# Optimization experiments

Hardware: AMD Instinct MI355X
Metric: run time of the kernel (lower is better)

Reference implementation:

```python
import jax, jax.numpy as jnp
import numpy as np

V, E, H, L = 10000, 300, 256, 9   # vocab, embed_dim, hidden_dim, num_labels
B, T = 128, 512                   # batch, seq_len


def setup_inputs() -> dict:
    key = jax.random.key(0)
    ks = jax.random.split(key, 14)
    s = 0.05
    emb = jax.random.normal(ks[2], (V, E), jnp.float32) * s
    emb = emb.at[0].set(0.0)  # padding_idx=0
    return {
        "input_ids": jax.random.randint(ks[0], (B, T), 0, V),
        "attention_mask": jnp.ones((B, T), jnp.int32),
        "labels": jax.random.randint(ks[1], (B, T), 0, L),
        "emb": emb,
        "Wih_f": jax.random.normal(ks[3], (4 * H, E), jnp.float32) * s,
        "Whh_f": jax.random.normal(ks[4], (4 * H, H), jnp.float32) * s,
        "b_f": jnp.zeros((4 * H,), jnp.float32),
        "Wih_b": jax.random.normal(ks[5], (4 * H, E), jnp.float32) * s,
        "Whh_b": jax.random.normal(ks[6], (4 * H, H), jnp.float32) * s,
        "b_b": jnp.zeros((4 * H,), jnp.float32),
        "Wc": jax.random.normal(ks[7], (L, 2 * H), jnp.float32) * s,
        "bc": jnp.zeros((L,), jnp.float32),
        "transitions": jax.random.normal(ks[8], (L, L), jnp.float32) * 0.1,
        "start_trans": jax.random.normal(ks[9], (L,), jnp.float32) * 0.1,
        "end_trans": jax.random.normal(ks[10], (L,), jnp.float32) * 0.1,
    }


def _lstm_dir(x, Wih, Whh, b):
    # x: (T, B, E) -> hidden states (T, B, H); PyTorch gate order i,f,g,o
    Bn = x.shape[1]
    h0 = jnp.zeros((Bn, Whh.shape[1]), x.dtype)
    c0 = jnp.zeros((Bn, Whh.shape[1]), x.dtype)
    # precompute input projections once (big GEMM), scan only does small HxH GEMM
    xp = jnp.einsum('tbe,ge->tbg', x, Wih) + b
    def step(carry, xg):
        h, c = carry
        g = xg + h @ Whh.T
        i, f, gg, o = jnp.split(g, 4, axis=-1)
        c = jax.nn.sigmoid(f) * c + jax.nn.sigmoid(i) * jnp.tanh(gg)
        h = jax.nn.sigmoid(o) * jnp.tanh(c)
        return (h, c), h
    _, hs = jax.lax.scan(step, (h0, c0), xp)
    return hs


def reference(input_ids, attention_mask, labels, emb, Wih_f, Whh_f, b_f,
              Wih_b, Whh_b, b_b, Wc, bc, transitions, start_trans, end_trans):
    x = emb[input_ids]                       # (B, T, E)
    xt = jnp.transpose(x, (1, 0, 2))         # (T, B, E)
    hf = _lstm_dir(xt, Wih_f, Whh_f, b_f)
    hb = _lstm_dir(xt[::-1], Wih_b, Whh_b, b_b)[::-1]
    h = jnp.concatenate([hf, hb], axis=-1)   # (T, B, 2H); dropout is identity in eval
    em = h @ Wc.T + bc                       # (T, B, L) emissions

    mask = jnp.transpose(attention_mask, (1, 0)).astype(bool)  # (T, B)
    tags = jnp.transpose(labels, (1, 0))                        # (T, B)
    Bn = em.shape[1]
    bidx = jnp.arange(Bn)

    # --- numerator: score of gold path (torchcrf._compute_score) ---
    score0 = start_trans[tags[0]] + em[0, bidx, tags[0]]
    def num_step(carry, inp):
        score, prev = carry
        e_t, t_t, m_t = inp
        score = score + (transitions[prev, t_t] + e_t[bidx, t_t]) * m_t
        return (score, t_t), None
    (score, _), _ = jax.lax.scan(
        num_step, (score0, tags[0]),
        (em[1:], tags[1:], mask[1:].astype(em.dtype)))
    seq_ends = mask.astype(jnp.int32).sum(0) - 1
    last_tags = tags[seq_ends, bidx]
    score = score + end_trans[last_tags]

    # --- denominator: log partition (torchcrf._compute_normalizer) ---
    alpha0 = start_trans + em[0]             # (B, L)
    def den_step(alpha, inp):
        e_t, m_t = inp
        nxt = jax.nn.logsumexp(alpha[:, :, None] + transitions[None] + e_t[:, None, :], axis=1)
        return jnp.where(m_t[:, None], nxt, alpha), None
    alpha, _ = jax.lax.scan(den_step, alpha0, (em[1:], mask[1:]))
    logZ = jax.nn.logsumexp(alpha + end_trans, axis=-1)

    llh = score - logZ
    return -jnp.mean(llh)  # crf(..., reduction='mean'), negated
```

## Files before the change

### kernel.cpp

```cpp
#include <hip/hip_runtime.h>
#include <hip/hip_bf16.h>
#include <hip/hip_fp16.h>

#define Vn 10000
#define En 300
#define E2n 150
#define Hn 256
#define Gn 1024
#define Ln 9
#define Bn 128
#define Tn 512

#if defined(__has_builtin)
#  if __has_builtin(__builtin_amdgcn_sdot8)
#    define HAS_SDOT8 1
#  endif
#  if __has_builtin(__builtin_amdgcn_fdot2)
#    define HAS_FDOT2 1
#  endif
#endif
#ifndef HAS_SDOT8
#  define HAS_SDOT8 0
#endif
#ifndef HAS_FDOT2
#  define HAS_FDOT2 0
#endif

typedef _Float16 half2_t __attribute__((ext_vector_type(2)));

static __device__ __forceinline__ float bf2f(unsigned short u) {
    return __uint_as_float(((unsigned int)u) << 16);
}
static __device__ __forceinline__ unsigned short f2bf(float f) {
    unsigned int x = __float_as_uint(f);
    return (unsigned short)((x + 0x7FFFu + ((x >> 16) & 1u)) >> 16);
}
static __device__ __forceinline__ float sigm(float x) {
    return 1.f / (1.f + __expf(-x));
}
static __device__ __forceinline__ float tanh_fast(float x) {
    return 2.f / (1.f + __expf(-2.f * x)) - 1.f;
}
static __device__ __forceinline__ int dot8(unsigned int w, int h, int acc) {
#if HAS_SDOT8
    return __builtin_amdgcn_sdot8((int)w, h, acc, false);
#else
    unsigned int wl = ((w & 0x0F0F0F0Fu) ^ 0x08080808u) - 0x08080808u;
    unsigned int wh = (((w >> 4) & 0x0F0F0F0Fu) ^ 0x08080808u) - 0x08080808u;
    unsigned int hl = (((unsigned)h & 0x0F0F0F0Fu) ^ 0x08080808u) - 0x08080808u;
    unsigned int hh = ((((unsigned)h >> 4) & 0x0F0F0F0Fu) ^ 0x08080808u) - 0x08080808u;
    acc = __builtin_amdgcn_sdot4((int)wl, (int)hl, acc, false);
    return __builtin_amdgcn_sdot4((int)wh, (int)hh, acc, false);
#endif
}
static __device__ __forceinline__ float fdot2f(unsigned int a, unsigned int b, float acc) {
#if HAS_FDOT2
    return __builtin_amdgcn_fdot2(__builtin_bit_cast(half2_t, a),
                                  __builtin_bit_cast(half2_t, b), acc, false);
#else
    half2_t av = __builtin_bit_cast(half2_t, a);
    half2_t bv = __builtin_bit_cast(half2_t, b);
    return acc + (float)av.x * (float)bv.x + (float)av.y * (float)bv.y;
#endif
}
static __device__ __forceinline__ unsigned int packf16(float a, float b) {
    half2_t v = {(_Float16)a, (_Float16)b};
    return __builtin_bit_cast(unsigned int, v);
}

__global__ __launch_bounds__(256) void k_prep_emb(
    const float* __restrict__ emb, unsigned int* __restrict__ embp) {
    int n = blockIdx.x * 256 + threadIdx.x;
    if (n >= Vn * E2n) return;
    int v = n / E2n, e2 = n % E2n;
    float a = emb[(size_t)v * En + 2 * e2];
    float b = emb[(size_t)v * En + 2 * e2 + 1];
    embp[n] = packf16(a, b);
}

__global__ __launch_bounds__(256) void k_prep_wt(
    const float* __restrict__ Wf, const float* __restrict__ Wb,
    unsigned int* __restrict__ Tf, unsigned int* __restrict__ Tb) {
    int n = blockIdx.x * 256 + threadIdx.x;
    const float* src = blockIdx.y ? Wb : Wf;
    unsigned int* dst = blockIdx.y ? Tb : Tf;
    int e2 = n / Gn, j = n % Gn;
    float a = src[(size_t)j * En + 2 * e2];
    float b = src[(size_t)j * En + 2 * e2 + 1];
    dst[n] = packf16(a, b);
}

__global__ __launch_bounds__(64) void k_quant_whh(
    const float* __restrict__ Wf, const float* __restrict__ Wb,
    unsigned int* __restrict__ qr_f, unsigned int* __restrict__ ql_f,
    unsigned int* __restrict__ qr_b, unsigned int* __restrict__ ql_b,
    float* __restrict__ scl_f, float* __restrict__ scl_b) {
    int j = blockIdx.x;
    int dir = blockIdx.y;
    int lane = threadIdx.x;
    const float* W = dir ? Wb : Wf;
    float w8[8];
    float m = 0.f;
    if (lane < 32) {
        float4 wlo = *(const float4*)&W[(size_t)j * Hn + 8 * lane];
        float4 whi = *(const float4*)&W[(size_t)j * Hn + 8 * lane + 4];
        w8[0] = wlo.x; w8[1] = wlo.y; w8[2] = wlo.z; w8[3] = wlo.w;
        w8[4] = whi.x; w8[5] = whi.y; w8[6] = whi.z; w8[7] = whi.w;
        #pragma unroll
        for (int i = 0; i < 8; ++i) m = fmaxf(m, fabsf(w8[i]));
    }
    #pragma unroll
    for (int sft = 32; sft >= 1; sft >>= 1) m = fmaxf(m, __shfl_xor(m, sft, 64));
    float inv = (m > 0.f) ? (7.f / m) : 0.f;
    if (lane < 32) {
        unsigned int d = 0;
        #pragma unroll
        for (int i = 0; i < 8; ++i) {
            int qi = (int)rintf(w8[i] * inv);
            d |= ((unsigned int)(qi & 0xF)) << (4 * i);
        }
        if (lane < 16)
            (dir ? qr_b : qr_f)[(size_t)((lane >> 2) * 1024 + j) * 4 + (lane & 3)] = d;
        else {
            int e = lane - 16;
            (dir ? ql_b : ql_f)[(size_t)((e >> 2) * 1024 + j) * 4 + (e & 3)] = d;
        }
    }
    if (lane == 0) (dir ? scl_b : scl_f)[j] = m / 49.f;
}

__global__ __launch_bounds__(256) void k_proj(
    const unsigned int* __restrict__ embp,
    const unsigned int* __restrict__ WT16_f, const unsigned int* __restrict__ WT16_b,
    const float* __restrict__ b_f, const float* __restrict__ b_b,
    unsigned short* __restrict__ Pf, unsigned short* __restrict__ Pb) {
    int tid = threadIdx.x;
    int tx = tid & 63, ty = tid >> 6;
    int dir = blockIdx.z;
    const unsigned int* WT = dir ? WT16_b : WT16_f;
    const float* bias = dir ? b_b : b_f;
    unsigned short* P = dir ? Pb : Pf;
    int v0 = blockIdx.x * 32 + ty * 8;
    int j0 = blockIdx.y * 256 + tx * 4;
    int vr[8];
    #pragma unroll
    for (int r = 0; r < 8; ++r) { int v = v0 + r; vr[r] = (v < Vn) ? v : Vn - 1; }
    float4 acc[8];
    #pragma unroll
    for (int r = 0; r < 8; ++r) acc[r] = make_float4(0.f, 0.f, 0.f, 0.f);
    for (int e2 = 0; e2 < E2n; ++e2) {
        uint4 w = *(const uint4*)&WT[(size_t)e2 * Gn + j0];
        #pragma unroll
        for (int r = 0; r < 8; ++r) {
            unsigned int a = embp[(size_t)vr[r] * E2n + e2];
            acc[r].x = fdot2f(a, w.x, acc[r].x);
            acc[r].y = fdot2f(a, w.y, acc[r].y);
            acc[r].z = fdot2f(a, w.z, acc[r].z);
            acc[r].w = fdot2f(a, w.w, acc[r].w);
        }
    }
    float4 bb = *(const float4*)&bias[j0];
    #pragma unroll
    for (int r = 0; r < 8; ++r) {
        if (v0 + r < Vn) {
            ushort4 o;
            o.x = f2bf(acc[r].x + bb.x); o.y = f2bf(acc[r].y + bb.y);
            o.z = f2bf(acc[r].z + bb.z); o.w = f2bf(acc[r].w + bb.w);
            *(ushort4*)&P[(size_t)(v0 + r) * Gn + j0] = o;
        }
    }
}

__global__ __launch_bounds__(1024, 4) void k_lstm(
    const int* __restrict__ ids,
    const uint4* __restrict__ qr_f, const uint4* __restrict__ ql_f,
    const uint4* __restrict__ qr_b, const uint4* __restrict__ ql_b,
    const float* __restrict__ scl_f, const float* __restrict__ scl_b,
    const unsigned short* __restrict__ Pf, const unsigned short* __restrict__ Pb,
    unsigned short* __restrict__ hs_f, unsigned short* __restrict__ hs_b) {
    __shared__ uint4 wlds[4 * 1024];
    __shared__ float g_stage[Gn];
    __shared__ uint4 h4v[8];
    __shared__ int ids_lds[Tn];
    int tid = threadIdx.x;
    int dir = blockIdx.x >> 7;
    int batch = blockIdx.x & 127;
    const uint4* qr = dir ? qr_b : qr_f;
    const uint4* ql = dir ? ql_b : ql_f;
    const unsigned short* P = dir ? Pb : Pf;
    unsigned short* hs = dir ? hs_b : hs_f;

    unsigned int wReg[16];
    #pragma unroll
    for (int d4 = 0; d4 < 4; ++d4) {
        uint4 v = qr[(size_t)d4 * 1024 + tid];
        wReg[4*d4+0] = v.x; wReg[4*d4+1] = v.y; wReg[4*d4+2] = v.z; wReg[4*d4+3] = v.w;
        wlds[d4 * 1024 + tid] = ql[(size_t)d4 * 1024 + tid];
    }
    float sc = (dir ? scl_b : scl_f)[tid];
    if (tid < Tn) ids_lds[tid] = ids[batch * Tn + tid];
    if (tid < 8) { uint4 z = {0u, 0u, 0u, 0u}; h4v[tid] = z; }
    float c = 0.f;
    __syncthreads();

    int t0 = dir ? (Tn - 1) : 0;
    float p = bf2f(P[(size_t)ids_lds[t0] * Gn + tid]);

    for (int s = 0; s < Tn; ++s) {
        asm volatile("" : "+v"(wReg[0]), "+v"(wReg[1]), "+v"(wReg[2]), "+v"(wReg[3]),
                          "+v"(wReg[4]), "+v"(wReg[5]), "+v"(wReg[6]), "+v"(wReg[7]),
                          "+v"(wReg[8]), "+v"(wReg[9]), "+v"(wReg[10]), "+v"(wReg[11]),
                          "+v"(wReg[12]), "+v"(wReg[13]), "+v"(wReg[14]), "+v"(wReg[15]));

        int t = dir ? (Tn - 1 - s) : s;
        int s2 = (s + 1 < Tn) ? s + 1 : Tn - 1;
        int t2 = dir ? (Tn - 1 - s2) : s2;
        unsigned short nx = P[(size_t)ids_lds[t2] * Gn + tid];

        uint4 hq  = h4v[tid & 7];
        uint4 wv0 = wlds[tid];
        uint4 wv1 = wlds[1024 + tid];
        uint4 wv2 = wlds[2048 + tid];
        uint4 wv3 = wlds[3072 + tid];

        int a0 = 0, a1 = 0, a2 = 0, a3 = 0;
        #pragma unroll
        for (int g = 0; g < 4; ++g) {
            int h0 = __builtin_amdgcn_readlane((int)hq.x, g);
            int h1 = __builtin_amdgcn_readlane((int)hq.y, g);
            int h2 = __builtin_amdgcn_readlane((int)hq.z, g);
            int h3 = __builtin_amdgcn_readlane((int)hq.w, g);
            a0 = dot8(wReg[4*g+0], h0, a0);
            a1 = dot8(wReg[4*g+1], h1, a1);
            a2 = dot8(wReg[4*g+2], h2, a2);
            a3 = dot8(wReg[4*g+3], h3, a3);
        }
        {
            uint4 wv[4] = {wv0, wv1, wv2, wv3};
            #pragma unroll
            for (int g = 4; g < 8; ++g) {
                int h0 = __builtin_amdgcn_readlane((int)hq.x, g);
                int h1 = __builtin_amdgcn_readlane((int)hq.y, g);
                int h2 = __builtin_amdgcn_readlane((int)hq.z, g);
                int h3 = __builtin_amdgcn_readlane((int)hq.w, g);
                a0 = dot8(wv[g-4].x, h0, a0);
                a1 = dot8(wv[g-4].y, h1, a1);
                a2 = dot8(wv[g-4].z, h2, a2);
                a3 = dot8(wv[g-4].w, h3, a3);
            }
        }
        g_stage[tid] = sc * (float)((a0 + a1) + (a2 + a3)) + p;
        __syncthreads();
        if (tid < Hn) {
            float gi = g_stage[tid];
            float gf = g_stage[tid + 256];
            float gg = g_stage[tid + 512];
            float go = g_stage[tid + 768];
            float cn = sigm(gf) * c + sigm(gi) * tanh_fast(gg);
            float hn = sigm(go) * tanh_fast(cn);
            c = cn;
            hs[(size_t)(t * Bn + batch) * Hn + tid] = f2bf(hn);
            int qh = (int)rintf(7.f * hn);
            int qo = __shfl_xor(qh, 1, 64);
            if ((tid & 1) == 0)
                ((char*)h4v)[tid >> 1] = (char)((qh & 0xF) | ((qo & 0xF) << 4));
        }
        __syncthreads();
        p = bf2f(nx);
    }
}

__global__ __launch_bounds__(256) void k_emit(
    const unsigned short* __restrict__ hs_f, const unsigned short* __restrict__ hs_b,
    const float* __restrict__ Wc, const float* __restrict__ bc,
    float* __restrict__ em) {
    __shared__ float wc_s[Ln * 2 * Hn];
    int tid = threadIdx.x;
    for (int i = tid; i < Ln * 2 * Hn; i += 256) wc_s[i] = Wc[i];
    __syncthreads();
    int lane = tid & 63, wid = tid >> 6;
    int tb = blockIdx.x * 4 + wid;
    const unsigned short* hf = hs_f + (size_t)tb * Hn;
    const unsigned short* hb = hs_b + (size_t)tb * Hn;
    uint2 uf = *(const uint2*)&hf[lane * 4];
    uint2 ub = *(const uint2*)&hb[lane * 4];
    float f0 = __uint_as_float(uf.x << 16), f1 = __uint_as_float(uf.x & 0xFFFF0000u);
    float f2v = __uint_as_float(uf.y << 16), f3 = __uint_as_float(uf.y & 0xFFFF0000u);
    float b0 = __uint_as_float(ub.x << 16), b1 = __uint_as_float(ub.x & 0xFFFF0000u);
    float b2 = __uint_as_float(ub.y << 16), b3 = __uint_as_float(ub.y & 0xFFFF0000u);
    #pragma unroll
    for (int l = 0; l < Ln; ++l) {
        const float* w = &wc_s[l * 2 * Hn];
        float p = f0 * w[4 * lane] + f1 * w[4 * lane + 1]
                + f2v * w[4 * lane + 2] + f3 * w[4 * lane + 3]
                + b0 * w[Hn + 4 * lane] + b1 * w[Hn + 4 * lane + 1]
                + b2 * w[Hn + 4 * lane + 2] + b3 * w[Hn + 4 * lane + 3];
        #pragma unroll
        for (int m = 32; m >= 1; m >>= 1) p += __shfl_xor(p, m, 64);
        if (lane == 0) em[(size_t)tb * Ln + l] = p + bc[l];
    }
}

__global__ __launch_bounds__(64) void k_crf_den(
    const float* __restrict__ em, const int* __restrict__ mask,
    const float* __restrict__ trans, const float* __restrict__ start,
    const float* __restrict__ endt, float* __restrict__ logZ) {
    int lane = threadIdx.x;
    int grp = lane >> 5;
    int b = blockIdx.x + 64 * grp;
    int lj = lane & 31;
    int jj = (lj < Ln) ? lj : Ln - 1;
    int base = lane & 32;
    float trj[Ln];
    #pragma unroll
    for (int i = 0; i < Ln; ++i) trj[i] = trans[i * Ln + jj];
    float alpha = start[jj] + em[(size_t)b * Ln + jj];
    float e1 = em[(size_t)(1 * Bn + b) * Ln + jj];
    float e2 = em[(size_t)(2 * Bn + b) * Ln + jj];
    int m1 = mask[b * Tn + 1];
    int m2 = mask[b * Tn + 2];
    for (int t = 1; t < Tn; ++t) {
        float s0 = __shfl(alpha, base + 0, 64) + trj[0];
        float s1 = __shfl(alpha, base + 1, 64) + trj[1];
        float s2 = __shfl(alpha, base + 2, 64) + trj[2];
        float s3 = __shfl(alpha, base + 3, 64) + trj[3];
        float s4 = __shfl(alpha, base + 4, 64) + trj[4];
        float s5 = __shfl(alpha, base + 5, 64) + trj[5];
        float s6 = __shfl(alpha, base + 6, 64) + trj[6];
        float s7 = __shfl(alpha, base + 7, 64) + trj[7];
        float s8 = __shfl(alpha, base + 8, 64) + trj[8];
        float mx = fmaxf(fmaxf(fmaxf(s0, s1), fmaxf(s2, s3)),
                         fmaxf(fmaxf(s4, s5), fmaxf(fmaxf(s6, s7), s8)));
        float sum = __expf(s0 - mx) + __expf(s1 - mx) + __expf(s2 - mx)
                  + __expf(s3 - mx) + __expf(s4 - mx) + __expf(s5 - mx)
                  + __expf(s6 - mx) + __expf(s7 - mx) + __expf(s8 - mx);
        float nxt = mx + __logf(sum) + e1;
        if (m1) alpha = nxt;
        e1 = e2; m1 = m2;
        int t2 = (t + 2 < Tn) ? t + 2 : Tn - 1;
        e2 = em[(size_t)(t2 * Bn + b) * Ln + jj];
        m2 = mask[b * Tn + t2];
    }
    float s = (lj < Ln) ? alpha + endt[lj] : -1e30f;
    float mx = s;
    #pragma unroll
    for (int d = 16; d >= 1; d >>= 1) mx = fmaxf(mx, __shfl_xor(mx, d, 64));
    float sm = __expf(s - mx);
    #pragma unroll
    for (int d = 16; d >= 1; d >>= 1) sm += __shfl_xor(sm, d, 64);
    if (lj == 0) logZ[b] = mx + __logf(sm);
}

__global__ __launch_bounds__(64) void k_crf_num(
    const float* __restrict__ em, const int* __restrict__ labels,
    const int* __restrict__ mask, const float* __restrict__ trans,
    const float* __restrict__ start, const float* __restrict__ endt,
    float* __restrict__ score) {
    int b = blockIdx.x, lane = threadIdx.x;
    float acc = 0.f; int cnt = 0;
    for (int t = lane; t < Tn; t += 64) {
        int tag = labels[b * Tn + t];
        int mt = mask[b * Tn + t];
        cnt += mt;
        float e = em[(size_t)(t * Bn + b) * Ln + tag];
        if (t == 0) {
            acc += start[tag] + e;
        } else {
            int prev = labels[b * Tn + t - 1];
            if (mt) acc += trans[prev * Ln + tag] + e;
        }
    }
    #pragma unroll
    for (int m = 32; m >= 1; m >>= 1) {
        acc += __shfl_xor(acc, m, 64);
        cnt += __shfl_xor(cnt, m, 64);
    }
    if (lane == 0) {
        int send = cnt - 1;
        int last = labels[b * Tn + send];
        score[b] = acc + endt[last];
    }
}

__global__ __launch_bounds__(128) void k_final(
    const float* __restrict__ score, const float* __restrict__ logZ,
    float* __restrict__ out) {
    __shared__ float s_s[128];
    int tid = threadIdx.x;
    s_s[tid] = score[tid] - logZ[tid];
    #pragma unroll
    for (int m = 64; m >= 1; m >>= 1) {
        __syncthreads();
        if (tid < m) s_s[tid] += s_s[tid + m];
    }
    if (tid == 0) out[0] = -s_s[0] / (float)Bn;
}

extern "C" void kernel_launch(void* const* d_in, const int* in_sizes, int n_in,
                              void* d_out, int out_size, void* d_ws, size_t ws_size,
                              hipStream_t stream) {
    const int* ids = (const int*)d_in[0];
    const int* msk = (const int*)d_in[1];
    const int* lbl = (const int*)d_in[2];
    const float* emb = (const float*)d_in[3];
    const float* Wih_f = (const float*)d_in[4];
    const float* Whh_f = (const float*)d_in[5];
    const float* b_f = (const float*)d_in[6];
    const float* Wih_b = (const float*)d_in[7];
    const float* Whh_b = (const float*)d_in[8];
    const float* b_b = (const float*)d_in[9];
    const float* Wc = (const float*)d_in[10];
    const float* bc = (const float*)d_in[11];
    const float* trans = (const float*)d_in[12];
    const float* st = (const float*)d_in[13];
    const float* en = (const float*)d_in[14];

    char* ws = (char*)d_ws;
    unsigned int* WT16_f = (unsigned int*)ws;   ws += (size_t)E2n * Gn * 4;
    unsigned int* WT16_b = (unsigned int*)ws;   ws += (size_t)E2n * Gn * 4;
    unsigned int* qr_f = (unsigned int*)ws;     ws += 65536;
    unsigned int* ql_f = (unsigned int*)ws;     ws += 65536;
    unsigned int* qr_b = (unsigned int*)ws;     ws += 65536;
    unsigned int* ql_b = (unsigned int*)ws;     ws += 65536;
    float* scl_f = (float*)ws;                  ws += 4096;
    float* scl_b = (float*)ws;                  ws += 4096;
    unsigned short* Pf = (unsigned short*)ws;   ws += (size_t)Vn * Gn * 2;
    unsigned short* Pb = (unsigned short*)ws;   ws += (size_t)Vn * Gn * 2;
    unsigned short* hs_f = (unsigned short*)ws; ws += (size_t)Tn * Bn * Hn * 2;
    unsigned short* hs_b = (unsigned short*)ws; ws += (size_t)Tn * Bn * Hn * 2;
    float* em = (float*)ws;                     ws += (size_t)Tn * Bn * Ln * 4;
    float* score = (float*)ws;                  ws += 512;
    float* logZ = (float*)ws;                   ws += 512;
    unsigned int* embp = (unsigned int*)hs_f;

    k_prep_emb<<<(Vn * E2n + 255) / 256, 256, 0, stream>>>(emb, embp);
    k_prep_wt<<<dim3((E2n * Gn) / 256, 2), 256, 0, stream>>>(Wih_f, Wih_b, WT16_f, WT16_b);
    k_quant_whh<<<dim3(1024, 2), 64, 0, stream>>>(Whh_f, Whh_b, qr_f, ql_f, qr_b, ql_b, scl_f, scl_b);
    k_proj<<<dim3(313, 4, 2), 256, 0, stream>>>(embp, WT16_f, WT16_b, b_f, b_b, Pf, Pb);
    k_lstm<<<256, 1024, 0, stream>>>(ids,
        (const uint4*)qr_f, (const uint4*)ql_f, (const uint4*)qr_b, (const uint4*)ql_b,
        scl_f, scl_b, Pf, Pb, hs_f, hs_b);
    k_emit<<<16384, 256, 0, stream>>>(hs_f, hs_b, Wc, bc, em);
    k_crf_den<<<64, 64, 0, stream>>>(em, msk, trans, st, en, logZ);
    k_crf_num<<<128, 64, 0, stream>>>(em, lbl, msk, trans, st, en, score);
    k_final<<<1, 128, 0, stream>>>(score, logZ, (float*)d_out);
}
```

Before: 929.3 us.

## Keep more int4 recurrent weights in registers and merge CRF numerator into denominator kernel

The register-resident share of the quantized Whh rows grows from 16 to 24 dwords per thread, and the LDS share shrinks from four uint4 slots to two, so each recurrent step issues fewer LDS reads on the serial LSTM critical path. The quantization kernel and workspace layout are changed to match the new split. Separately, the CRF numerator is computed by otherwise idle lanes (lj>=16) inside the denominator kernel, which removes one kernel launch. The cost is higher VGPR pressure at 1024 threads per block, which could cause spills, and a longer prologue in the CRF kernel.

```diff
diff --git a/kernel.cpp b/kernel.cpp
--- a/kernel.cpp
+++ b/kernel.cpp
@@ -119,10 +119,10 @@
             int qi = (int)rintf(w8[i] * inv);
             d |= ((unsigned int)(qi & 0xF)) << (4 * i);
         }
-        if (lane < 16)
+        if (lane < 24)
             (dir ? qr_b : qr_f)[(size_t)((lane >> 2) * 1024 + j) * 4 + (lane & 3)] = d;
         else {
-            int e = lane - 16;
+            int e = lane - 24;
             (dir ? ql_b : ql_f)[(size_t)((e >> 2) * 1024 + j) * 4 + (e & 3)] = d;
         }
     }
@@ -178,7 +178,7 @@
     const float* __restrict__ scl_f, const float* __restrict__ scl_b,
     const unsigned short* __restrict__ Pf, const unsigned short* __restrict__ Pb,
     unsigned short* __restrict__ hs_f, unsigned short* __restrict__ hs_b) {
-    __shared__ uint4 wlds[4 * 1024];
+    __shared__ uint4 wlds[2 * 1024];
     __shared__ float g_stage[Gn];
     __shared__ uint4 h4v[8];
     __shared__ int ids_lds[Tn];
@@ -190,13 +190,14 @@
     const unsigned short* P = dir ? Pb : Pf;
     unsigned short* hs = dir ? hs_b : hs_f;
 
-    unsigned int wReg[16];
-    #pragma unroll
-    for (int d4 = 0; d4 < 4; ++d4) {
+    unsigned int wReg[24];
+    #pragma unroll
+    for (int d4 = 0; d4 < 6; ++d4) {
         uint4 v = qr[(size_t)d4 * 1024 + tid];
         wReg[4*d4+0] = v.x; wReg[4*d4+1] = v.y; wReg[4*d4+2] = v.z; wReg[4*d4+3] = v.w;
-        wlds[d4 * 1024 + tid] = ql[(size_t)d4 * 1024 + tid];
-    }
+    }
+    wlds[tid] = ql[tid];
+    wlds[1024 + tid] = ql[1024 + tid];
     float sc = (dir ? scl_b : scl_f)[tid];
     if (tid < Tn) ids_lds[tid] = ids[batch * Tn + tid];
     if (tid < 8) { uint4 z = {0u, 0u, 0u, 0u}; h4v[tid] = z; }
@@ -209,8 +210,10 @@
     for (int s = 0; s < Tn; ++s) {
         asm volatile("" : "+v"(wReg[0]), "+v"(wReg[1]), "+v"(wReg[2]), "+v"(wReg[3]),
                           "+v"(wReg[4]), "+v"(wReg[5]), "+v"(wReg[6]), "+v"(wReg[7]),
-                          "+v"(wReg[8]), "+v"(wReg[9]), "+v"(wReg[10]), "+v"(wReg[11]),
-                          "+v"(wReg[12]), "+v"(wReg[13]), "+v"(wReg[14]), "+v"(wReg[15]));
+                          "+v"(wReg[8]), "+v"(wReg[9]), "+v"(wReg[10]), "+v"(wReg[11]));
+        asm volatile("" : "+v"(wReg[12]), "+v"(wReg[13]), "+v"(wReg[14]), "+v"(wReg[15]),
+                          "+v"(wReg[16]), "+v"(wReg[17]), "+v"(wReg[18]), "+v"(wReg[19]),
+                          "+v"(wReg[20]), "+v"(wReg[21]), "+v"(wReg[22]), "+v"(wReg[23]));
 
         int t = dir ? (Tn - 1 - s) : s;
         int s2 = (s + 1 < Tn) ? s + 1 : Tn - 1;
@@ -220,12 +223,10 @@
         uint4 hq  = h4v[tid & 7];
         uint4 wv0 = wlds[tid];
         uint4 wv1 = wlds[1024 + tid];
-        uint4 wv2 = wlds[2048 + tid];
-        uint4 wv3 = wlds[3072 + tid];
 
         int a0 = 0, a1 = 0, a2 = 0, a3 = 0;
         #pragma unroll
-        for (int g = 0; g < 4; ++g) {
+        for (int g = 0; g < 6; ++g) {
             int h0 = __builtin_amdgcn_readlane((int)hq.x, g);
             int h1 = __builtin_amdgcn_readlane((int)hq.y, g);
             int h2 = __builtin_amdgcn_readlane((int)hq.z, g);
@@ -236,18 +237,22 @@
             a3 = dot8(wReg[4*g+3], h3, a3);
         }
         {
-            uint4 wv[4] = {wv0, wv1, wv2, wv3};
-            #pragma unroll
-            for (int g = 4; g < 8; ++g) {
-                int h0 = __builtin_amdgcn_readlane((int)hq.x, g);
-                int h1 = __builtin_amdgcn_readlane((int)hq.y, g);
-                int h2 = __builtin_amdgcn_readlane((int)hq.z, g);
-                int h3 = __builtin_amdgcn_readlane((int)hq.w, g);
-                a0 = dot8(wv[g-4].x, h0, a0);
-                a1 = dot8(wv[g-4].y, h1, a1);
-                a2 = dot8(wv[g-4].z, h2, a2);
-                a3 = dot8(wv[g-4].w, h3, a3);
-            }
+            int h0 = __builtin_amdgcn_readlane((int)hq.x, 6);
+            int h1 = __builtin_amdgcn_readlane((int)hq.y, 6);
+            int h2 = __builtin_amdgcn_readlane((int)hq.z, 6);
+            int h3 = __builtin_amdgcn_readlane((int)hq.w, 6);
+            a0 = dot8(wv0.x, h0, a0);
+            a1 = dot8(wv0.y, h1, a1);
+            a2 = dot8(wv0.z, h2, a2);
+            a3 = dot8(wv0.w, h3, a3);
+            h0 = __builtin_amdgcn_readlane((int)hq.x, 7);
+            h1 = __builtin_amdgcn_readlane((int)hq.y, 7);
+            h2 = __builtin_amdgcn_readlane((int)hq.z, 7);
+            h3 = __builtin_amdgcn_readlane((int)hq.w, 7);
+            a0 = dot8(wv1.x, h0, a0);
+            a1 = dot8(wv1.y, h1, a1);
+            a2 = dot8(wv1.z, h2, a2);
+            a3 = dot8(wv1.w, h3, a3);
         }
         g_stage[tid] = sc * (float)((a0 + a1) + (a2 + a3)) + p;
         __syncthreads();
@@ -301,10 +306,11 @@
     }
 }
 
-__global__ __launch_bounds__(64) void k_crf_den(
-    const float* __restrict__ em, const int* __restrict__ mask,
-    const float* __restrict__ trans, const float* __restrict__ start,
-    const float* __restrict__ endt, float* __restrict__ logZ) {
+__global__ __launch_bounds__(64) void k_crf(
+    const float* __restrict__ em, const int* __restrict__ labels,
+    const int* __restrict__ mask, const float* __restrict__ trans,
+    const float* __restrict__ start, const float* __restrict__ endt,
+    float* __restrict__ score, float* __restrict__ logZ) {
     int lane = threadIdx.x;
     int grp = lane >> 5;
     int b = blockIdx.x + 64 * grp;
@@ -319,6 +325,26 @@
     float e2 = em[(size_t)(2 * Bn + b) * Ln + jj];
     int m1 = mask[b * Tn + 1];
     int m2 = mask[b * Tn + 2];
+
+    float nacc = 0.f; int ncnt = 0;
+    bool numlane = (lj >= 16);
+    if (numlane) {
+        int tq = lj - 16;
+        for (int k = 0; k < Tn / 16; ++k) {
+            int t = tq + 16 * k;
+            int tag = labels[b * Tn + t];
+            int mt = mask[b * Tn + t];
+            ncnt += mt;
+            float e = em[(size_t)(t * Bn + b) * Ln + tag];
+            if (t == 0) {
+                nacc += start[tag] + e;
+            } else {
+                int prev = labels[b * Tn + t - 1];
+                if (mt) nacc += trans[prev * Ln + tag] + e;
+            }
+        }
+    }
+
     for (int t = 1; t < Tn; ++t) {
         float s0 = __shfl(alpha, base + 0, 64) + trj[0];
         float s1 = __shfl(alpha, base + 1, 64) + trj[1];
@@ -349,36 +375,16 @@
     #pragma unroll
     for (int d = 16; d >= 1; d >>= 1) sm += __shfl_xor(sm, d, 64);
     if (lj == 0) logZ[b] = mx + __logf(sm);
-}
-
-__global__ __launch_bounds__(64) void k_crf_num(
-    const float* __restrict__ em, const int* __restrict__ labels,
-    const int* __restrict__ mask, const float* __restrict__ trans,
-    const float* __restrict__ start, const float* __restrict__ endt,
-    float* __restrict__ score) {
-    int b = blockIdx.x, lane = threadIdx.x;
-    float acc = 0.f; int cnt = 0;
-    for (int t = lane; t < Tn; t += 64) {
-        int tag = labels[b * Tn + t];
-        int mt = mask[b * Tn + t];
-        cnt += mt;
-        float e = em[(size_t)(t * Bn + b) * Ln + tag];
-        if (t == 0) {
-            acc += start[tag] + e;
-        } else {
-            int prev = labels[b * Tn + t - 1];
-            if (mt) acc += trans[prev * Ln + tag] + e;
-        }
-    }
-    #pragma unroll
-    for (int m = 32; m >= 1; m >>= 1) {
-        acc += __shfl_xor(acc, m, 64);
-        cnt += __shfl_xor(cnt, m, 64);
-    }
-    if (lane == 0) {
-        int send = cnt - 1;
+    if (!numlane) { nacc = 0.f; ncnt = 0; }
+    #pragma unroll
+    for (int d = 8; d >= 1; d >>= 1) {
+        nacc += __shfl_xor(nacc, d, 64);
+        ncnt += __shfl_xor(ncnt, d, 64);
+    }
+    if (lj == 16) {
+        int send = ncnt - 1;
         int last = labels[b * Tn + send];
-        score[b] = acc + endt[last];
+        score[b] = nacc + endt[last];
     }
 }
 
@@ -418,10 +424,10 @@
     char* ws = (char*)d_ws;
     unsigned int* WT16_f = (unsigned int*)ws;   ws += (size_t)E2n * Gn * 4;
     unsigned int* WT16_b = (unsigned int*)ws;   ws += (size_t)E2n * Gn * 4;
-    unsigned int* qr_f = (unsigned int*)ws;     ws += 65536;
-    unsigned int* ql_f = (unsigned int*)ws;     ws += 65536;
-    unsigned int* qr_b = (unsigned int*)ws;     ws += 65536;
-    unsigned int* ql_b = (unsigned int*)ws;     ws += 65536;
+    unsigned int* qr_f = (unsigned int*)ws;     ws += 98304;
+    unsigned int* ql_f = (unsigned int*)ws;     ws += 32768;
+    unsigned int* qr_b = (unsigned int*)ws;     ws += 98304;
+    unsigned int* ql_b = (unsigned int*)ws;     ws += 32768;
     float* scl_f = (float*)ws;                  ws += 4096;
     float* scl_b = (float*)ws;                  ws += 4096;
     unsigned short* Pf = (unsigned short*)ws;   ws += (size_t)Vn * Gn * 2;
@@ -441,7 +447,6 @@
         (const uint4*)qr_f, (const uint4*)ql_f, (const uint4*)qr_b, (const uint4*)ql_b,
         scl_f, scl_b, Pf, Pb, hs_f, hs_b);
     k_emit<<<16384, 256, 0, stream>>>(hs_f, hs_b, Wc, bc, em);
-    k_crf_den<<<64, 64, 0, stream>>>(em, msk, trans, st, en, logZ);
-    k_crf_num<<<128, 64, 0, stream>>>(em, lbl, msk, trans, st, en, score);
+    k_crf<<<64, 64, 0, stream>>>(em, lbl, msk, trans, st, en, score, logZ);
     k_final<<<1, 128, 0, stream>>>(score, logZ, (float*)d_out);
 }
```

Result: no change. 947.5 us (+2.0%).

## Restructure LSTM step so each thread computes all four gates via quad shuffles

Applied to the files above, without the earlier changes.

The recurrent step is remapped so four lanes share one hidden unit. Each lane dot-products a quarter of the hidden vector for all four gates, then the partial sums are reduced with xor shuffles. This removes the g_stage LDS round-trip and one __syncthreads per timestep, keeps three gates' weights in registers (24 VGPRs) with only the output gate in LDS, and packs the new h into double-buffered LDS words via shuffles. The weight quantization layout changes to match, and the projection kernel is unrolled by two over the embedding dimension. The cost is higher register pressure, extra shuffles, and only one lane in four doing the nonlinearity.

```diff
diff --git a/kernel.cpp b/kernel.cpp
--- a/kernel.cpp
+++ b/kernel.cpp
@@ -119,12 +119,13 @@
             int qi = (int)rintf(w8[i] * inv);
             d |= ((unsigned int)(qi & 0xF)) << (4 * i);
         }
-        if (lane < 16)
-            (dir ? qr_b : qr_f)[(size_t)((lane >> 2) * 1024 + j) * 4 + (lane & 3)] = d;
-        else {
-            int e = lane - 16;
-            (dir ? ql_b : ql_f)[(size_t)((e >> 2) * 1024 + j) * 4 + (e & 3)] = d;
-        }
+        int u = j & 255, g = j >> 8;
+        int kq = lane >> 3, half = (lane >> 2) & 1, sub = lane & 3;
+        int tid = 4 * u + kq;
+        if (g < 3)
+            (dir ? qr_b : qr_f)[(size_t)((g * 2 + half) * 1024 + tid) * 4 + sub] = d;
+        else
+            (dir ? ql_b : ql_f)[(size_t)(half * 1024 + tid) * 4 + sub] = d;
     }
     if (lane == 0) (dir ? scl_b : scl_f)[j] = m / 49.f;
 }
@@ -148,15 +149,20 @@
     float4 acc[8];
     #pragma unroll
     for (int r = 0; r < 8; ++r) acc[r] = make_float4(0.f, 0.f, 0.f, 0.f);
-    for (int e2 = 0; e2 < E2n; ++e2) {
-        uint4 w = *(const uint4*)&WT[(size_t)e2 * Gn + j0];
+    for (int e2 = 0; e2 < E2n; e2 += 2) {
+        uint4 w0 = *(const uint4*)&WT[(size_t)(e2 + 0) * Gn + j0];
+        uint4 w1 = *(const uint4*)&WT[(size_t)(e2 + 1) * Gn + j0];
         #pragma unroll
         for (int r = 0; r < 8; ++r) {
-            unsigned int a = embp[(size_t)vr[r] * E2n + e2];
-            acc[r].x = fdot2f(a, w.x, acc[r].x);
-            acc[r].y = fdot2f(a, w.y, acc[r].y);
-            acc[r].z = fdot2f(a, w.z, acc[r].z);
-            acc[r].w = fdot2f(a, w.w, acc[r].w);
+            uint2 a = *(const uint2*)&embp[(size_t)vr[r] * E2n + e2];
+            acc[r].x = fdot2f(a.x, w0.x, acc[r].x);
+            acc[r].y = fdot2f(a.x, w0.y, acc[r].y);
+            acc[r].z = fdot2f(a.x, w0.z, acc[r].z);
+            acc[r].w = fdot2f(a.x, w0.w, acc[r].w);
+            acc[r].x = fdot2f(a.y, w1.x, acc[r].x);
+            acc[r].y = fdot2f(a.y, w1.y, acc[r].y);
+            acc[r].z = fdot2f(a.y, w1.z, acc[r].z);
+            acc[r].w = fdot2f(a.y, w1.w, acc[r].w);
         }
     }
     float4 bb = *(const float4*)&bias[j0];
@@ -178,95 +184,106 @@
     const float* __restrict__ scl_f, const float* __restrict__ scl_b,
     const unsigned short* __restrict__ Pf, const unsigned short* __restrict__ Pb,
     unsigned short* __restrict__ hs_f, unsigned short* __restrict__ hs_b) {
-    __shared__ uint4 wlds[4 * 1024];
-    __shared__ float g_stage[Gn];
-    __shared__ uint4 h4v[8];
+    __shared__ uint4 wlds[2 * 1024];
+    __shared__ unsigned int h4q[2][32];
     __shared__ int ids_lds[Tn];
     int tid = threadIdx.x;
     int dir = blockIdx.x >> 7;
     int batch = blockIdx.x & 127;
+    int u = tid >> 2, kq = tid & 3;
     const uint4* qr = dir ? qr_b : qr_f;
     const uint4* ql = dir ? ql_b : ql_f;
     const unsigned short* P = dir ? Pb : Pf;
     unsigned short* hs = dir ? hs_b : hs_f;
 
-    unsigned int wReg[16];
-    #pragma unroll
-    for (int d4 = 0; d4 < 4; ++d4) {
-        uint4 v = qr[(size_t)d4 * 1024 + tid];
-        wReg[4*d4+0] = v.x; wReg[4*d4+1] = v.y; wReg[4*d4+2] = v.z; wReg[4*d4+3] = v.w;
-        wlds[d4 * 1024 + tid] = ql[(size_t)d4 * 1024 + tid];
-    }
-    float sc = (dir ? scl_b : scl_f)[tid];
+    unsigned int wReg[24];
+    #pragma unroll
+    for (int d6 = 0; d6 < 6; ++d6) {
+        uint4 v = qr[(size_t)d6 * 1024 + tid];
+        wReg[4*d6+0] = v.x; wReg[4*d6+1] = v.y; wReg[4*d6+2] = v.z; wReg[4*d6+3] = v.w;
+    }
+    wlds[tid] = ql[tid];
+    wlds[1024 + tid] = ql[1024 + tid];
+    float myscl = (dir ? scl_b : scl_f)[u + 256 * kq];
+    float sc0 = myscl;
+    float sc1 = __shfl_xor(myscl, 1, 64);
+    float sc2 = __shfl_xor(myscl, 2, 64);
+    float sc3 = __shfl_xor(myscl, 3, 64);
     if (tid < Tn) ids_lds[tid] = ids[batch * Tn + tid];
-    if (tid < 8) { uint4 z = {0u, 0u, 0u, 0u}; h4v[tid] = z; }
+    if (tid < 32) h4q[0][tid] = 0u;
     float c = 0.f;
     __syncthreads();
 
     int t0 = dir ? (Tn - 1) : 0;
-    float p = bf2f(P[(size_t)ids_lds[t0] * Gn + tid]);
+    unsigned short pcur = P[(size_t)ids_lds[t0] * Gn + u + 256 * kq];
 
     for (int s = 0; s < Tn; ++s) {
         asm volatile("" : "+v"(wReg[0]), "+v"(wReg[1]), "+v"(wReg[2]), "+v"(wReg[3]),
                           "+v"(wReg[4]), "+v"(wReg[5]), "+v"(wReg[6]), "+v"(wReg[7]),
-                          "+v"(wReg[8]), "+v"(wReg[9]), "+v"(wReg[10]), "+v"(wReg[11]),
-                          "+v"(wReg[12]), "+v"(wReg[13]), "+v"(wReg[14]), "+v"(wReg[15]));
+                          "+v"(wReg[8]), "+v"(wReg[9]), "+v"(wReg[10]), "+v"(wReg[11]));
+        asm volatile("" : "+v"(wReg[12]), "+v"(wReg[13]), "+v"(wReg[14]), "+v"(wReg[15]),
+                          "+v"(wReg[16]), "+v"(wReg[17]), "+v"(wReg[18]), "+v"(wReg[19]),
+                          "+v"(wReg[20]), "+v"(wReg[21]), "+v"(wReg[22]), "+v"(wReg[23]));
 
         int t = dir ? (Tn - 1 - s) : s;
+        int cur = s & 1;
         int s2 = (s + 1 < Tn) ? s + 1 : Tn - 1;
         int t2 = dir ? (Tn - 1 - s2) : s2;
-        unsigned short nx = P[(size_t)ids_lds[t2] * Gn + tid];
-
-        uint4 hq  = h4v[tid & 7];
-        uint4 wv0 = wlds[tid];
-        uint4 wv1 = wlds[1024 + tid];
-        uint4 wv2 = wlds[2048 + tid];
-        uint4 wv3 = wlds[3072 + tid];
+        unsigned short pnx = P[(size_t)ids_lds[t2] * Gn + u + 256 * kq];
+
+        const uint4* hb = (const uint4*)&h4q[cur][kq * 8];
+        uint4 h0 = hb[0], h1 = hb[1];
+        uint4 wo0 = wlds[tid], wo1 = wlds[1024 + tid];
 
         int a0 = 0, a1 = 0, a2 = 0, a3 = 0;
-        #pragma unroll
-        for (int g = 0; g < 4; ++g) {
-            int h0 = __builtin_amdgcn_readlane((int)hq.x, g);
-            int h1 = __builtin_amdgcn_readlane((int)hq.y, g);
-            int h2 = __builtin_amdgcn_readlane((int)hq.z, g);
-            int h3 = __builtin_amdgcn_readlane((int)hq.w, g);
-            a0 = dot8(wReg[4*g+0], h0, a0);
-            a1 = dot8(wReg[4*g+1], h1, a1);
-            a2 = dot8(wReg[4*g+2], h2, a2);
-            a3 = dot8(wReg[4*g+3], h3, a3);
-        }
-        {
-            uint4 wv[4] = {wv0, wv1, wv2, wv3};
-            #pragma unroll
-            for (int g = 4; g < 8; ++g) {
-                int h0 = __builtin_amdgcn_readlane((int)hq.x, g);
-                int h1 = __builtin_amdgcn_readlane((int)hq.y, g);
-                int h2 = __builtin_amdgcn_readlane((int)hq.z, g);
-                int h3 = __builtin_amdgcn_readlane((int)hq.w, g);
-                a0 = dot8(wv[g-4].x, h0, a0);
-                a1 = dot8(wv[g-4].y, h1, a1);
-                a2 = dot8(wv[g-4].z, h2, a2);
-                a3 = dot8(wv[g-4].w, h3, a3);
-            }
-        }
-        g_stage[tid] = sc * (float)((a0 + a1) + (a2 + a3)) + p;
-        __syncthreads();
-        if (tid < Hn) {
-            float gi = g_stage[tid];
-            float gf = g_stage[tid + 256];
-            float gg = g_stage[tid + 512];
-            float go = g_stage[tid + 768];
+        a0 = dot8(wReg[0], (int)h0.x, a0);  a0 = dot8(wReg[1], (int)h0.y, a0);
+        a0 = dot8(wReg[2], (int)h0.z, a0);  a0 = dot8(wReg[3], (int)h0.w, a0);
+        a0 = dot8(wReg[4], (int)h1.x, a0);  a0 = dot8(wReg[5], (int)h1.y, a0);
+        a0 = dot8(wReg[6], (int)h1.z, a0);  a0 = dot8(wReg[7], (int)h1.w, a0);
+        a1 = dot8(wReg[8], (int)h0.x, a1);  a1 = dot8(wReg[9], (int)h0.y, a1);
+        a1 = dot8(wReg[10], (int)h0.z, a1); a1 = dot8(wReg[11], (int)h0.w, a1);
+        a1 = dot8(wReg[12], (int)h1.x, a1); a1 = dot8(wReg[13], (int)h1.y, a1);
+        a1 = dot8(wReg[14], (int)h1.z, a1); a1 = dot8(wReg[15], (int)h1.w, a1);
+        a2 = dot8(wReg[16], (int)h0.x, a2); a2 = dot8(wReg[17], (int)h0.y, a2);
+        a2 = dot8(wReg[18], (int)h0.z, a2); a2 = dot8(wReg[19], (int)h0.w, a2);
+        a2 = dot8(wReg[20], (int)h1.x, a2); a2 = dot8(wReg[21], (int)h1.y, a2);
+        a2 = dot8(wReg[22], (int)h1.z, a2); a2 = dot8(wReg[23], (int)h1.w, a2);
+        a3 = dot8(wo0.x, (int)h0.x, a3);    a3 = dot8(wo0.y, (int)h0.y, a3);
+        a3 = dot8(wo0.z, (int)h0.z, a3);    a3 = dot8(wo0.w, (int)h0.w, a3);
+        a3 = dot8(wo1.x, (int)h1.x, a3);    a3 = dot8(wo1.y, (int)h1.y, a3);
+        a3 = dot8(wo1.z, (int)h1.z, a3);    a3 = dot8(wo1.w, (int)h1.w, a3);
+
+        a0 += __shfl_xor(a0, 1, 64); a0 += __shfl_xor(a0, 2, 64);
+        a1 += __shfl_xor(a1, 1, 64); a1 += __shfl_xor(a1, 2, 64);
+        a2 += __shfl_xor(a2, 1, 64); a2 += __shfl_xor(a2, 2, 64);
+        a3 += __shfl_xor(a3, 1, 64); a3 += __shfl_xor(a3, 2, 64);
+
+        float pv = bf2f(pcur);
+        float p1 = __shfl_xor(pv, 1, 64);
+        float p2 = __shfl_xor(pv, 2, 64);
+        float p3 = __shfl_xor(pv, 3, 64);
+
+        int qh = 0;
+        if (kq == 0) {
+            float gi = sc0 * (float)a0 + pv;
+            float gf = sc1 * (float)a1 + p1;
+            float gg = sc2 * (float)a2 + p2;
+            float go = sc3 * (float)a3 + p3;
             float cn = sigm(gf) * c + sigm(gi) * tanh_fast(gg);
             float hn = sigm(go) * tanh_fast(cn);
             c = cn;
-            hs[(size_t)(t * Bn + batch) * Hn + tid] = f2bf(hn);
-            int qh = (int)rintf(7.f * hn);
-            int qo = __shfl_xor(qh, 1, 64);
-            if ((tid & 1) == 0)
-                ((char*)h4v)[tid >> 1] = (char)((qh & 0xF) | ((qo & 0xF) << 4));
+            hs[(size_t)(t * Bn + batch) * Hn + u] = f2bf(hn);
+            qh = (int)rintf(7.f * hn) & 0xF;
         }
+        int o1 = __shfl_xor(qh, 4, 64);
+        int b8 = qh | (o1 << 4);
+        int o2 = __shfl_xor(b8, 8, 64);
+        int b16 = (b8 & 0xFF) | ((o2 & 0xFF) << 8);
+        int o3 = __shfl_xor(b16, 16, 64);
+        unsigned int b32 = (unsigned int)((b16 & 0xFFFF) | (o3 << 16));
+        if ((tid & 31) == 0) h4q[cur ^ 1][tid >> 5] = b32;
         __syncthreads();
-        p = bf2f(nx);
+        pcur = pnx;
     }
 }
 
@@ -418,10 +435,10 @@
     char* ws = (char*)d_ws;
     unsigned int* WT16_f = (unsigned int*)ws;   ws += (size_t)E2n * Gn * 4;
     unsigned int* WT16_b = (unsigned int*)ws;   ws += (size_t)E2n * Gn * 4;
-    unsigned int* qr_f = (unsigned int*)ws;     ws += 65536;
-    unsigned int* ql_f = (unsigned int*)ws;     ws += 65536;
-    unsigned int* qr_b = (unsigned int*)ws;     ws += 65536;
-    unsigned int* ql_b = (unsigned int*)ws;     ws += 65536;
+    unsigned int* qr_f = (unsigned int*)ws;     ws += 98304;
+    unsigned int* ql_f = (unsigned int*)ws;     ws += 32768;
+    unsigned int* qr_b = (unsigned int*)ws;     ws += 98304;
+    unsigned int* ql_b = (unsigned int*)ws;     ws += 32768;
     float* scl_f = (float*)ws;                  ws += 4096;
     float* scl_b = (float*)ws;                  ws += 4096;
     unsigned short* Pf = (unsigned short*)ws;   ws += (size_t)Vn * Gn * 2;
```

Measured after the change: 1.135 ms. +22.2%, slower.
